# Kernel tuning notes

Measured on AMD Instinct MI355X. Metric: run time of the kernel, lower is better.

## Reference

```python
import jax, jax.numpy as jnp
import numpy as np

N_NODES = 50000
N_RELS = 8
IN_DIM = 128
OUT_DIM = 128
N_EDGES = 800000


def setup_inputs() -> dict:
    key = jax.random.key(0)
    k1, k2, k3, k4 = jax.random.split(key, 4)
    src = jax.random.randint(k1, (N_EDGES,), 0, N_NODES, dtype=jnp.int64 if jax.config.jax_enable_x64 else jnp.int32)
    rel = jax.random.randint(k2, (N_EDGES,), 0, N_RELS, dtype=src.dtype)
    tgt = jax.random.randint(k3, (N_EDGES,), 0, N_NODES, dtype=src.dtype)
    triples = jnp.stack([src, rel, tgt], axis=1)  # (E, 3) like torch layout (s, r, t)
    features = jax.random.normal(k4, (N_NODES, IN_DIM), dtype=jnp.float32)
    weights = jax.random.normal(jax.random.fold_in(key, 1), (N_RELS, IN_DIM, OUT_DIM), dtype=jnp.float32) * (1.0 / np.sqrt(IN_DIM))
    bias = jnp.zeros((OUT_DIM,), dtype=jnp.float32)
    return {"triples": triples, "features": features, "weights": weights, "bias": bias}


def reference(triples, features, weights, bias):
    # RGCN-NC forward, horizontal stacking (featured mode):
    #   out[t] = sum_{(s,r,t) in E} (1/c_{t,r}) * features[s] @ W[r] + bias
    # where c_{t,r} = #edges sharing the same (relation, target) pair,
    # matching sum_sparse(..., row_normalisation=False) on the (n x r*n) adjacency.
    src, rel, tgt = triples[:, 0], triples[:, 1], triples[:, 2]
    n = features.shape[0]
    r = weights.shape[0]
    e = triples.shape[0]

    # per-(rel, tgt) edge counts -> 1/c normalization per edge
    key = rel * n + tgt  # column index of horizontally stacked adjacency
    counts = jax.ops.segment_sum(jnp.ones((e,), dtype=features.dtype), key, num_segments=r * n)
    vals = 1.0 / counts[key]  # (E,)

    # dense per-relation transform: H[r] = X @ W[r]   (r, n, out)
    h = jnp.einsum('ni,rio->rno', features, weights)

    # gather per-edge messages, scale, scatter-add into targets
    msgs = h[rel, src] * vals[:, None]  # (E, out)
    out = jax.ops.segment_sum(msgs, tgt, num_segments=n)  # (n, out)
    return out + bias
```

## Files before the change

kernel.cpp:

```cpp
#include <hip/hip_runtime.h>
#include <hip/hip_bf16.h>

#define N_NODES 50000
#define N_RELS 8
#define IN_DIM 128
#define OUT_DIM 128
#define N_EDGES 800000
#define KDIM (N_RELS * IN_DIM)
#define CAP 64
#define FUSE_BLKS 1563
#define EG_BLKS ((N_EDGES / 4 + 255) / 256)
#define CW_BLKS ((N_RELS * IN_DIM * OUT_DIM + 255) / 256)
#define FB_BLKS ((N_NODES * IN_DIM / 8 + 255) / 256)

typedef __attribute__((ext_vector_type(8))) short bf16x8;
typedef __attribute__((ext_vector_type(4))) float floatx4;
typedef __attribute__((ext_vector_type(4))) unsigned int uintx4;

__device__ inline unsigned short f2bf(float f) {
    unsigned u = __builtin_bit_cast(unsigned, f);
    u += 0x7fff + ((u >> 16) & 1);
    return (unsigned short)(u >> 16);
}
__device__ inline float bflo(unsigned u) {
    return __builtin_bit_cast(float, u << 16);
}
__device__ inline float bfhi(unsigned u) {
    return __builtin_bit_cast(float, u & 0xffff0000u);
}

__global__ void prep2_kernel(const int* __restrict__ tri, const float* __restrict__ W,
                             const float* __restrict__ features,
                             int* __restrict__ bcnt, int* __restrict__ bdata,
                             unsigned short* __restrict__ Wtf,
                             unsigned short* __restrict__ featB) {
    const int b = blockIdx.x;
    if (b < EG_BLKS) {
        int t = b * 256 + threadIdx.x;
        if (t >= N_EDGES / 4) return;
        const int4* tri4 = (const int4*)tri;
        int4 a = tri4[3 * t], v = tri4[3 * t + 1], c = tri4[3 * t + 2];
        int s[4] = { a.x, a.w, v.z, c.y };
        int r[4] = { a.y, v.x, v.w, c.z };
        int g[4] = { a.z, v.y, c.x, c.w };
#pragma unroll
        for (int k = 0; k < 4; ++k) {
            const int pos = atomicAdd(&bcnt[g[k]], 1);
            if (pos < CAP) bdata[g[k] * CAP + pos] = s[k] | (r[k] << 16);
        }
    } else if (b < EG_BLKS + CW_BLKS) {
        int idx = (b - EG_BLKS) * 256 + threadIdx.x;
        if (idx >= N_RELS * IN_DIM * OUT_DIM) return;
        int e  = idx & 7;
        int l  = (idx >> 3) & 63;
        int ks = (idx >> 9) & 31;
        int nt = idx >> 14;
        int o = nt * 16 + (l & 15);
        int k = ks * 32 + (l >> 4) * 8 + e;
        Wtf[idx] = f2bf(W[(k >> 7) * (IN_DIM * OUT_DIM) + (k & 127) * OUT_DIM + o]);
    } else {
        int t = (b - EG_BLKS - CW_BLKS) * 256 + threadIdx.x;
        if (t >= N_NODES * IN_DIM / 8) return;
        const float4* f4 = (const float4*)features;
        float4 x = f4[2 * t], y = f4[2 * t + 1];
        uint4 o;
        o.x = (unsigned)f2bf(x.x) | ((unsigned)f2bf(x.y) << 16);
        o.y = (unsigned)f2bf(x.z) | ((unsigned)f2bf(x.w) << 16);
        o.z = (unsigned)f2bf(y.x) | ((unsigned)f2bf(y.y) << 16);
        o.w = (unsigned)f2bf(y.z) | ((unsigned)f2bf(y.w) << 16);
        ((uint4*)featB)[t] = o;
    }
}

__global__ __launch_bounds__(512, 8) void fused_kernel(
    const int* __restrict__ bcnt, const int* __restrict__ bdata,
    const unsigned short* __restrict__ featB,
    const unsigned short* __restrict__ Wtf,
    const float* __restrict__ bias,
    float* __restrict__ out)
{
    __shared__ __align__(16) unsigned short Atile[32 * 512];
    __shared__ unsigned short srcS[2048];
    __shared__ int cntL[256];
    __shared__ int segL[256];
    __shared__ int curL[256];
    __shared__ int cntN[32];

    const int tid = threadIdx.x;
    const int b = blockIdx.x;
    const int wave = tid >> 6, lane = tid & 63;
    const int q = lane >> 4, l16 = lane & 15;
    const int m0 = b * 32;
    const int wm = wave & 1, wn = wave >> 1;

    if (tid < 32) {
        const int node = m0 + tid;
        int c = (node < N_NODES) ? bcnt[node] : 0;
        cntN[tid] = (c > CAP) ? CAP : c;
    }
    if (tid < 256) cntL[tid] = 0;
    __syncthreads();
    {
        const int nl = tid >> 4;
        const int node = m0 + nl;
        const int cn = cntN[nl];
        for (int j = tid & 15; j < cn; j += 16) {
            const unsigned u = (unsigned)bdata[node * CAP + j];
            atomicAdd(&cntL[nl * 8 + ((u >> 16) & 7)], 1);
        }
    }
    __syncthreads();
    if (tid < 256) segL[tid] = cntL[tid];
    __syncthreads();
    for (int off = 1; off < 256; off <<= 1) {
        int x = 0;
        if (tid < 256 && tid >= off) x = segL[tid - off];
        __syncthreads();
        if (tid < 256) segL[tid] += x;
        __syncthreads();
    }
    if (tid < 256) {
        const int ex = segL[tid] - cntL[tid];
        segL[tid] = ex;
        curL[tid] = ex;
    }
    __syncthreads();
    {
        const int nl = tid >> 4;
        const int node = m0 + nl;
        const int cn = cntN[nl];
        for (int j = tid & 15; j < cn; j += 16) {
            const unsigned u = (unsigned)bdata[node * CAP + j];
            const int pos = atomicAdd(&curL[nl * 8 + ((u >> 16) & 7)], 1);
            srcS[pos] = (unsigned short)(u & 0xffff);
        }
    }
    __syncthreads();

    floatx4 acc[2];
#pragma unroll
    for (int nt = 0; nt < 2; ++nt) acc[nt] = (floatx4){0.f, 0.f, 0.f, 0.f};

    const unsigned short* fb = featB + 8 * l16;

#pragma unroll
    for (int p = 0; p < 2; ++p) {
        for (int i = 0; i < 4; ++i) {
            const int nl = wave * 4 + i;
            const int key = nl * 8 + 4 * p + q;
            const int s0 = segL[key];
            const int len = cntL[key];
            float a0 = 0.f, a1 = 0.f, a2 = 0.f, a3 = 0.f;
            float a4 = 0.f, a5 = 0.f, a6 = 0.f, a7 = 0.f;
            for (int j = 0; j < len; j += 2) {
                const int sa = srcS[s0 + j];
                const int jb = (j + 1 < len) ? (j + 1) : j;
                const int sb = srcS[s0 + jb];
                const bool pb = j + 1 < len;
                uint4 ua = *(const uint4*)&fb[sa * IN_DIM];
                uint4 ub = *(const uint4*)&fb[sb * IN_DIM];
                a0 += bflo(ua.x); a1 += bfhi(ua.x);
                a2 += bflo(ua.y); a3 += bfhi(ua.y);
                a4 += bflo(ua.z); a5 += bfhi(ua.z);
                a6 += bflo(ua.w); a7 += bfhi(ua.w);
                if (pb) {
                    a0 += bflo(ub.x); a1 += bfhi(ub.x);
                    a2 += bflo(ub.y); a3 += bfhi(ub.y);
                    a4 += bflo(ub.z); a5 += bfhi(ub.z);
                    a6 += bflo(ub.w); a7 += bfhi(ub.w);
                }
            }
            const float inv = (len > 0) ? 1.0f / (float)len : 0.0f;
            uintx4 pk;
            pk[0] = (unsigned)f2bf(a0 * inv) | ((unsigned)f2bf(a1 * inv) << 16);
            pk[1] = (unsigned)f2bf(a2 * inv) | ((unsigned)f2bf(a3 * inv) << 16);
            pk[2] = (unsigned)f2bf(a4 * inv) | ((unsigned)f2bf(a5 * inv) << 16);
            pk[3] = (unsigned)f2bf(a6 * inv) | ((unsigned)f2bf(a7 * inv) << 16);
            const int us = (q * 16 + l16) ^ (nl & 15);
            *(uintx4*)&Atile[(nl * 64 + us) * 8] = pk;
        }
        __syncthreads();

        __builtin_amdgcn_s_setprio(1);
#pragma unroll
        for (int ksl = 0; ksl < 16; ++ksl) {
            const int ks = p * 16 + ksl;
            const int r = wm * 16 + l16;
            const int us = (ksl * 4 + q) ^ (r & 15);
            bf16x8 a = *(const bf16x8*)&Atile[(r * 64 + us) * 8];
#pragma unroll
            for (int nt = 0; nt < 2; ++nt) {
                const int ntg = wn * 2 + nt;
                bf16x8 bb = *(const bf16x8*)&Wtf[(size_t)((ntg * 32 + ks) * 64 + lane) * 8];
                acc[nt] = __builtin_amdgcn_mfma_f32_16x16x32_bf16(a, bb, acc[nt], 0, 0, 0);
            }
        }
        __builtin_amdgcn_s_setprio(0);
        __syncthreads();
    }

    float* fbuf = (float*)Atile;
#pragma unroll
    for (int nt = 0; nt < 2; ++nt) {
        const int o = (wn * 2 + nt) * 16 + l16;
        const float bv = bias[o];
#pragma unroll
        for (int j = 0; j < 4; ++j) {
            const int r = wm * 16 + q * 4 + j;
            fbuf[r * 128 + o] = acc[nt][j] + bv;
        }
    }
    __syncthreads();
    {
        const int row = tid >> 4;
        const int col = (tid & 15) * 8;
        const int node = m0 + row;
        if (node < N_NODES) {
            floatx4 w0 = *(const floatx4*)&fbuf[row * 128 + col];
            floatx4 w1 = *(const floatx4*)&fbuf[row * 128 + col + 4];
            float* po = &out[(size_t)node * OUT_DIM + col];
            __builtin_nontemporal_store(w0, (floatx4*)po);
            __builtin_nontemporal_store(w1, (floatx4*)(po + 4));
        }
    }
}

extern "C" void kernel_launch(void* const* d_in, const int* in_sizes, int n_in,
                              void* d_out, int out_size, void* d_ws, size_t ws_size,
                              hipStream_t stream)
{
    const int*   tri      = (const int*)d_in[0];
    const float* features = (const float*)d_in[1];
    const float* W        = (const float*)d_in[2];
    const float* bias     = (const float*)d_in[3];
    float* out = (float*)d_out;

    char* ws = (char*)d_ws;
    unsigned short* Wtf = (unsigned short*)ws; ws += (size_t)OUT_DIM * KDIM * 2;
    int* bcnt  = (int*)ws; ws += (size_t)50048 * 4;
    int* bdata = (int*)ws; ws += (size_t)N_NODES * CAP * 4;
    unsigned short* featB = (unsigned short*)ws; ws += (size_t)N_NODES * IN_DIM * 2;
    (void)ws_size; (void)in_sizes; (void)n_in; (void)out_size;

    hipMemsetAsync(bcnt, 0, 50048 * sizeof(int), stream);
    prep2_kernel<<<EG_BLKS + CW_BLKS + FB_BLKS, 256, 0, stream>>>(
        tri, W, features, bcnt, bdata, Wtf, featB);
    fused_kernel<<<FUSE_BLKS, 512, 0, stream>>>(bcnt, bdata, featB, Wtf, bias, out);
}
```

Measured before the change: 226.8 us.

## Vectorize bucket load, use wave-shuffle scan, interleave two node gathers

The per-block bucketing now loads each node's edge entries with one vectorized uint4 load per thread and replaces the shared-memory Hillis-Steele scan, which had many barriers, with a wave-level shuffle scan plus a small cross-wave fixup. The gather loop processes two nodes at once, issuing four independent feature loads per iteration to raise memory-level parallelism, at the cost of wasted predicated loads when the two lengths differ. The epilogue's float staging buffer gets a padded stride to reduce LDS bank conflicts. Reading all 64 slots per node (past the count) relies on the bdata buffer being fully allocated for the last block.

Result: no change. 230.5 us (+1.6%).

```diff
diff --git a/kernel.cpp b/kernel.cpp
--- a/kernel.cpp
+++ b/kernel.cpp
@@ -12,6 +12,7 @@
 #define EG_BLKS ((N_EDGES / 4 + 255) / 256)
 #define CW_BLKS ((N_RELS * IN_DIM * OUT_DIM + 255) / 256)
 #define FB_BLKS ((N_NODES * IN_DIM / 8 + 255) / 256)
+#define FB_STRIDE 132
 
 typedef __attribute__((ext_vector_type(8))) short bf16x8;
 typedef __attribute__((ext_vector_type(4))) float floatx4;
@@ -84,7 +85,8 @@
     __shared__ int cntL[256];
     __shared__ int segL[256];
     __shared__ int curL[256];
-    __shared__ int cntN[32];
+    __shared__ int cnN[32];
+    __shared__ int wpart[4];
 
     const int tid = threadIdx.x;
     const int b = blockIdx.x;
@@ -96,43 +98,54 @@
     if (tid < 32) {
         const int node = m0 + tid;
         int c = (node < N_NODES) ? bcnt[node] : 0;
-        cntN[tid] = (c > CAP) ? CAP : c;
+        cnN[tid] = (c > CAP) ? CAP : c;
     }
     if (tid < 256) cntL[tid] = 0;
-    __syncthreads();
-    {
-        const int nl = tid >> 4;
-        const int node = m0 + nl;
-        const int cn = cntN[nl];
-        for (int j = tid & 15; j < cn; j += 16) {
-            const unsigned u = (unsigned)bdata[node * CAP + j];
-            atomicAdd(&cntL[nl * 8 + ((u >> 16) & 7)], 1);
-        }
-    }
-    __syncthreads();
-    if (tid < 256) segL[tid] = cntL[tid];
-    __syncthreads();
-    for (int off = 1; off < 256; off <<= 1) {
-        int x = 0;
-        if (tid < 256 && tid >= off) x = segL[tid - off];
-        __syncthreads();
-        if (tid < 256) segL[tid] += x;
-        __syncthreads();
-    }
-    if (tid < 256) {
-        const int ex = segL[tid] - cntL[tid];
-        segL[tid] = ex;
-        curL[tid] = ex;
-    }
-    __syncthreads();
-    {
-        const int nl = tid >> 4;
-        const int node = m0 + nl;
-        const int cn = cntN[nl];
-        for (int j = tid & 15; j < cn; j += 16) {
-            const unsigned u = (unsigned)bdata[node * CAP + j];
-            const int pos = atomicAdd(&curL[nl * 8 + ((u >> 16) & 7)], 1);
-            srcS[pos] = (unsigned short)(u & 0xffff);
+    if (tid == 0) srcS[0] = 0;
+    __syncthreads();
+
+    const uint4 eq = ((const uint4*)(bdata + (size_t)m0 * CAP))[tid];
+    int ent[4] = { (int)eq.x, (int)eq.y, (int)eq.z, (int)eq.w };
+    const int slot0 = tid * 4;
+#pragma unroll
+    for (int k = 0; k < 4; ++k) {
+        const int nl = (slot0 + k) >> 6;
+        const int jj = (slot0 + k) & 63;
+        if (jj < cnN[nl]) atomicAdd(&cntL[nl * 8 + ((ent[k] >> 16) & 7)], 1);
+    }
+    __syncthreads();
+
+    int vkey = 0, vinc = 0;
+    if (wave < 4) {
+        const int key = wave * 64 + lane;
+        vkey = cntL[key];
+        vinc = vkey;
+#pragma unroll
+        for (int off = 1; off < 64; off <<= 1) {
+            int t2 = __shfl_up(vinc, off);
+            if (lane >= off) vinc += t2;
+        }
+        if (lane == 63) wpart[wave] = vinc;
+    }
+    __syncthreads();
+    if (wave < 4) {
+        const int key = wave * 64 + lane;
+        int pre = 0;
+#pragma unroll
+        for (int w2 = 0; w2 < 3; ++w2) if (w2 < wave) pre += wpart[w2];
+        const int ex = vinc - vkey + pre;
+        segL[key] = ex;
+        curL[key] = ex;
+    }
+    __syncthreads();
+
+#pragma unroll
+    for (int k = 0; k < 4; ++k) {
+        const int nl = (slot0 + k) >> 6;
+        const int jj = (slot0 + k) & 63;
+        if (jj < cnN[nl]) {
+            const int pos = atomicAdd(&curL[nl * 8 + ((ent[k] >> 16) & 7)], 1);
+            srcS[pos] = (unsigned short)(ent[k] & 0xffff);
         }
     }
     __syncthreads();
@@ -145,39 +158,67 @@
 
 #pragma unroll
     for (int p = 0; p < 2; ++p) {
-        for (int i = 0; i < 4; ++i) {
-            const int nl = wave * 4 + i;
-            const int key = nl * 8 + 4 * p + q;
-            const int s0 = segL[key];
-            const int len = cntL[key];
-            float a0 = 0.f, a1 = 0.f, a2 = 0.f, a3 = 0.f;
-            float a4 = 0.f, a5 = 0.f, a6 = 0.f, a7 = 0.f;
-            for (int j = 0; j < len; j += 2) {
-                const int sa = srcS[s0 + j];
-                const int jb = (j + 1 < len) ? (j + 1) : j;
-                const int sb = srcS[s0 + jb];
-                const bool pb = j + 1 < len;
-                uint4 ua = *(const uint4*)&fb[sa * IN_DIM];
-                uint4 ub = *(const uint4*)&fb[sb * IN_DIM];
-                a0 += bflo(ua.x); a1 += bfhi(ua.x);
-                a2 += bflo(ua.y); a3 += bfhi(ua.y);
-                a4 += bflo(ua.z); a5 += bfhi(ua.z);
-                a6 += bflo(ua.w); a7 += bfhi(ua.w);
-                if (pb) {
-                    a0 += bflo(ub.x); a1 += bfhi(ub.x);
-                    a2 += bflo(ub.y); a3 += bfhi(ub.y);
-                    a4 += bflo(ub.z); a5 += bfhi(ub.z);
-                    a6 += bflo(ub.w); a7 += bfhi(ub.w);
+#pragma unroll
+        for (int ii = 0; ii < 4; ii += 2) {
+            const int nlA = wave * 4 + ii, nlB = nlA + 1;
+            const int keyA = nlA * 8 + 4 * p + q;
+            const int keyB = keyA + 8;
+            const int sA = segL[keyA], lA = cntL[keyA];
+            const int sB = segL[keyB], lB = cntL[keyB];
+            const int jm = (lA > lB) ? lA : lB;
+            float a0=0.f,a1=0.f,a2=0.f,a3=0.f,a4=0.f,a5=0.f,a6=0.f,a7=0.f;
+            float b0=0.f,b1=0.f,b2=0.f,b3=0.f,b4=0.f,b5=0.f,b6=0.f,b7=0.f;
+            for (int j = 0; j < jm; j += 2) {
+                const bool pA0 = j < lA,     pA1 = j + 1 < lA;
+                const bool pB0 = j < lB,     pB1 = j + 1 < lB;
+                const int iA0 = pA0 ? (sA + j)     : 0;
+                const int iA1 = pA1 ? (sA + j + 1) : 0;
+                const int iB0 = pB0 ? (sB + j)     : 0;
+                const int iB1 = pB1 ? (sB + j + 1) : 0;
+                uint4 uA0 = *(const uint4*)&fb[srcS[iA0] * IN_DIM];
+                uint4 uA1 = *(const uint4*)&fb[srcS[iA1] * IN_DIM];
+                uint4 uB0 = *(const uint4*)&fb[srcS[iB0] * IN_DIM];
+                uint4 uB1 = *(const uint4*)&fb[srcS[iB1] * IN_DIM];
+                if (pA0) {
+                    a0 += bflo(uA0.x); a1 += bfhi(uA0.x);
+                    a2 += bflo(uA0.y); a3 += bfhi(uA0.y);
+                    a4 += bflo(uA0.z); a5 += bfhi(uA0.z);
+                    a6 += bflo(uA0.w); a7 += bfhi(uA0.w);
+                }
+                if (pA1) {
+                    a0 += bflo(uA1.x); a1 += bfhi(uA1.x);
+                    a2 += bflo(uA1.y); a3 += bfhi(uA1.y);
+                    a4 += bflo(uA1.z); a5 += bfhi(uA1.z);
+                    a6 += bflo(uA1.w); a7 += bfhi(uA1.w);
+                }
+                if (pB0) {
+                    b0 += bflo(uB0.x); b1 += bfhi(uB0.x);
+                    b2 += bflo(uB0.y); b3 += bfhi(uB0.y);
+                    b4 += bflo(uB0.z); b5 += bfhi(uB0.z);
+                    b6 += bflo(uB0.w); b7 += bfhi(uB0.w);
+                }
+                if (pB1) {
+                    b0 += bflo(uB1.x); b1 += bfhi(uB1.x);
+                    b2 += bflo(uB1.y); b3 += bfhi(uB1.y);
+                    b4 += bflo(uB1.z); b5 += bfhi(uB1.z);
+                    b6 += bflo(uB1.w); b7 += bfhi(uB1.w);
                 }
             }
-            const float inv = (len > 0) ? 1.0f / (float)len : 0.0f;
-            uintx4 pk;
-            pk[0] = (unsigned)f2bf(a0 * inv) | ((unsigned)f2bf(a1 * inv) << 16);
-            pk[1] = (unsigned)f2bf(a2 * inv) | ((unsigned)f2bf(a3 * inv) << 16);
-            pk[2] = (unsigned)f2bf(a4 * inv) | ((unsigned)f2bf(a5 * inv) << 16);
-            pk[3] = (unsigned)f2bf(a6 * inv) | ((unsigned)f2bf(a7 * inv) << 16);
-            const int us = (q * 16 + l16) ^ (nl & 15);
-            *(uintx4*)&Atile[(nl * 64 + us) * 8] = pk;
+            const float invA = (lA > 0) ? 1.0f / (float)lA : 0.0f;
+            const float invB = (lB > 0) ? 1.0f / (float)lB : 0.0f;
+            uintx4 pkA, pkB;
+            pkA[0] = (unsigned)f2bf(a0 * invA) | ((unsigned)f2bf(a1 * invA) << 16);
+            pkA[1] = (unsigned)f2bf(a2 * invA) | ((unsigned)f2bf(a3 * invA) << 16);
+            pkA[2] = (unsigned)f2bf(a4 * invA) | ((unsigned)f2bf(a5 * invA) << 16);
+            pkA[3] = (unsigned)f2bf(a6 * invA) | ((unsigned)f2bf(a7 * invA) << 16);
+            pkB[0] = (unsigned)f2bf(b0 * invB) | ((unsigned)f2bf(b1 * invB) << 16);
+            pkB[1] = (unsigned)f2bf(b2 * invB) | ((unsigned)f2bf(b3 * invB) << 16);
+            pkB[2] = (unsigned)f2bf(b4 * invB) | ((unsigned)f2bf(b5 * invB) << 16);
+            pkB[3] = (unsigned)f2bf(b6 * invB) | ((unsigned)f2bf(b7 * invB) << 16);
+            const int usA = (q * 16 + l16) ^ (nlA & 15);
+            const int usB = (q * 16 + l16) ^ (nlB & 15);
+            *(uintx4*)&Atile[(nlA * 64 + usA) * 8] = pkA;
+            *(uintx4*)&Atile[(nlB * 64 + usB) * 8] = pkB;
         }
         __syncthreads();
 
@@ -207,7 +248,7 @@
 #pragma unroll
         for (int j = 0; j < 4; ++j) {
             const int r = wm * 16 + q * 4 + j;
-            fbuf[r * 128 + o] = acc[nt][j] + bv;
+            fbuf[r * FB_STRIDE + o] = acc[nt][j] + bv;
         }
     }
     __syncthreads();
@@ -216,8 +257,8 @@
         const int col = (tid & 15) * 8;
         const int node = m0 + row;
         if (node < N_NODES) {
-            floatx4 w0 = *(const floatx4*)&fbuf[row * 128 + col];
-            floatx4 w1 = *(const floatx4*)&fbuf[row * 128 + col + 4];
+            floatx4 w0 = *(const floatx4*)&fbuf[row * FB_STRIDE + col];
+            floatx4 w1 = *(const floatx4*)&fbuf[row * FB_STRIDE + col + 4];
             float* po = &out[(size_t)node * OUT_DIM + col];
             __builtin_nontemporal_store(w0, (floatx4*)po);
             __builtin_nontemporal_store(w1, (floatx4*)(po + 4));
```
